# Kernel optimization log

Hardware: AMD Instinct MI355X
Metric: run time of the kernel (lower is better)

## Reference

```python
import jax, jax.numpy as jnp
import numpy as np

KEEP_RATIO = 0.3
ALPHA, BETA, GAMMA, SMOOTH = 0.3, 0.7, 1.33, 1e-6
LOVASZ_W = 0.2


def _bce_with_logits(x, t):
    # stable binary_cross_entropy_with_logits, reduction='none'
    return jnp.maximum(x, 0.0) - x * t + jnp.log1p(jnp.exp(-jnp.abs(x)))


def _ohem_image(loss_i, tgt_i, tis_i, k_all):
    # loss_i/tgt_i/tis_i: [P] per-image flattened
    P = loss_i.shape[0]
    pos = tgt_i * tis_i                       # 1.0 where kept positive
    n_pos = jnp.sum(pos).astype(jnp.int32)
    neg_mask = (tgt_i == 0) & (tis_i == 1)
    n_remain = jnp.maximum(0, k_all - n_pos)
    # top-n_remain negative losses via full descending sort + rank mask
    neg_vals = jnp.where(neg_mask, loss_i, -jnp.inf)
    neg_sorted = -jnp.sort(-neg_vals)         # descending
    ranks = jnp.arange(P)
    valid = (ranks < n_remain) & jnp.isfinite(neg_sorted)
    neg_sum = jnp.sum(jnp.where(valid, neg_sorted, 0.0))
    n_neg_kept = jnp.sum(valid).astype(jnp.int32)
    pos_sum = jnp.sum(loss_i * pos)
    cnt = n_pos + n_neg_kept
    # fallback when nothing kept: hardest pixel inside tissue (or pixel 0)
    tis_vals = jnp.where(tis_i == 1, loss_i, -jnp.inf)
    has_tissue = jnp.any(tis_i == 1)
    fallback = jnp.where(has_tissue, jnp.max(tis_vals), loss_i[0])
    return jnp.where(cnt > 0, (pos_sum + neg_sum) / jnp.maximum(cnt, 1), fallback)


def _lovasz_image(log_flat, lab_flat):
    # binary Lovasz hinge, per image
    signs = 2.0 * lab_flat - 1.0
    errors = 1.0 - log_flat * signs
    order = jnp.argsort(-errors)              # descending by error
    errors_sorted = errors[order]
    gt_sorted = lab_flat[order]
    p = jnp.sum(gt_sorted)
    intersection = p - jnp.cumsum(gt_sorted)
    union = p + jnp.cumsum(1.0 - gt_sorted)
    jaccard = 1.0 - intersection / union
    n = gt_sorted.shape[0] - p
    grad = jnp.where(n > 0,
                     jnp.concatenate([jaccard[:1], jaccard[1:] - jaccard[:-1]]),
                     jaccard)
    return jnp.dot(jax.nn.relu(errors_sorted), grad)


def _forward(logits, targets, tissue_mask):
    t = targets.astype(jnp.float32)
    B = logits.shape[0]
    lf = logits.reshape(B, -1)                # [B, P]
    tf = t.reshape(B, -1)
    mf = tissue_mask.reshape(B, -1)
    P = lf.shape[1]
    k_all = max(1, int(P * KEEP_RATIO))       # static

    # --- OHEM BCE ---
    bce = _bce_with_logits(lf, tf) * mf
    ohem_i = jax.vmap(lambda l, tg, ms: _ohem_image(l, tg, ms, k_all))(bce, tf, mf)
    ohem_term = jnp.mean(ohem_i)

    # --- focal Tversky (per image) ---
    probs = jax.nn.sigmoid(lf)
    tp = jnp.sum(probs * tf, axis=1)
    fn = jnp.sum((1.0 - probs) * tf, axis=1)
    fp = jnp.sum(probs * (1.0 - tf), axis=1)
    tversky = (tp + SMOOTH) / (tp + ALPHA * fn + BETA * fp + SMOOTH)
    ft_i = (1.0 - tversky) ** GAMMA

    # --- Lovasz hinge (per image) ---
    lov_i = jax.vmap(_lovasz_image)(lf, tf)

    # masked mean over images that contain positives
    posb = jnp.sum(tf, axis=1) > 0
    npos = jnp.sum(posb)
    denom = jnp.maximum(npos, 1).astype(lf.dtype)
    ft_term = jnp.sum(jnp.where(posb, ft_i, 0.0)) / denom
    lov_term = jnp.sum(jnp.where(posb, lov_i, 0.0)) / denom
    return ohem_term + jnp.where(npos > 0, ft_term + LOVASZ_W * lov_term, 0.0)


def setup_inputs() -> dict:
    key = jax.random.key(0)
    k1, k2 = jax.random.split(key)
    B, H, W = 16, 768, 768
    logits = jax.random.normal(k1, (B, 1, H, W), dtype=jnp.float32)
    targets = jax.random.randint(k2, (B, 1, H, W), 0, 2, dtype=jnp.int32)
    tissue_mask = jnp.ones((B, 1, H, W), dtype=jnp.float32)
    return {"logits": logits, "targets": targets, "tissue_mask": tissue_mask}


def reference(logits, targets, tissue_mask):
    return _forward(logits, targets, tissue_mask)
```

## Files before the change

kernel.cpp:

```cpp
#include <hip/hip_runtime.h>
#include <math.h>

#define BB 16
#define PP (768*768)
#define NBINS 4096
#define CHUNKS 64
#define KALL 176947

#define LOV_LO (-17.0f)
#define LOV_RANGE 34.0f

typedef unsigned long long u64;

struct PAcc { float pos_sum, pos_w, tpx, sprx, mx, sum_t, n_tis, bce0; };
struct AccR { float lov_i, ft_i, ohem_i; unsigned posb; };

__device__ inline float wred_sum(float v) {
  #pragma unroll
  for (int o = 32; o > 0; o >>= 1) v += __shfl_down(v, o, 64);
  return v;
}
__device__ inline float wred_max(float v) {
  #pragma unroll
  for (int o = 32; o > 0; o >>= 1) v = fmaxf(v, __shfl_down(v, o, 64));
  return v;
}

__global__ __launch_bounds__(256) void k_main(const float* __restrict__ logits,
                                              const int* __restrict__ targets,
                                              const float* __restrict__ mask,
                                              PAcc* __restrict__ pacc,
                                              u64* __restrict__ partial)
{
  const int b = blockIdx.y;
  const int chunk = blockIdx.x;
  __shared__ unsigned hist1[NBINS];
  __shared__ unsigned hist2[NBINS];
  __shared__ float wsum[4][8];
  for (int i = threadIdx.x; i < NBINS; i += 256) { hist1[i] = 0u; hist2[i] = 0u; }
  __syncthreads();

  const float4* l4 = (const float4*)(logits + (size_t)b * PP);
  const int4*   t4 = (const int4*)(targets + (size_t)b * PP);
  const float4* m4 = (const float4*)(mask + (size_t)b * PP);

  const float lov_scale = (float)NBINS / LOV_RANGE;

  float pos_sum = 0.f, pos_w = 0.f, tpa = 0.f, spra = 0.f, mx = 0.f;
  float sum_t = 0.f, n_tis = 0.f, bce0 = 0.f;

  if (chunk == 0 && threadIdx.x == 0) {
    float l = logits[(size_t)b * PP];
    float tf = (float)targets[(size_t)b * PP];
    float m = mask[(size_t)b * PP];
    float ex = __expf(-fabsf(l));
    bce0 = (fmaxf(l, 0.f) + __logf(1.f + ex) - l * tf) * m;
  }

  const int per_chunk4 = (PP / CHUNKS) / 4;
  const int base4 = chunk * per_chunk4;
  const int iters = per_chunk4 / 256;

  for (int it = 0; it < iters; ++it) {
    int i = base4 + it * 256 + threadIdx.x;
    float4 lv = l4[i]; int4 tv = t4[i]; float4 mv = m4[i];
    float ls[4] = {lv.x, lv.y, lv.z, lv.w};
    int   ts[4] = {tv.x, tv.y, tv.z, tv.w};
    float ms[4] = {mv.x, mv.y, mv.z, mv.w};
    #pragma unroll
    for (int c = 0; c < 4; ++c) {
      float l = ls[c]; int ti = ts[c]; float tf = (float)ti; float m = ms[c];
      float ex = __expf(-fabsf(l));
      float lg = __logf(1.f + ex);
      float loss = (fmaxf(l, 0.f) + lg - l * tf) * m;
      float posw = tf * m;
      pos_sum = fmaf(loss, posw, pos_sum);
      pos_w  += posw;
      float pr = ((l >= 0.f) ? 1.f : ex) * __builtin_amdgcn_rcpf(1.f + ex);
      spra += pr;
      tpa = fmaf(pr, tf, tpa);
      sum_t += tf;
      bool tis = (m == 1.0f);
      if (tis) { n_tis += 1.f; mx = fmaxf(mx, loss); }
      float s = fmaf(2.f, tf, -1.f);
      float e = fmaf(-l, s, 1.f);
      int bin = (int)((e - LOV_LO) * lov_scale);
      bin = bin < 0 ? 0 : (bin > NBINS - 1 ? NBINS - 1 : bin);
      atomicAdd(&hist1[bin], 1u | ((unsigned)ti << 16));
      if ((ti == 0) & tis) atomicAdd(&hist2[bin], 1u);
    }
  }

  {
    float v0 = wred_sum(pos_sum), v1 = wred_sum(pos_w), v2 = wred_sum(tpa);
    float v3 = wred_sum(spra), v4 = wred_max(mx), v5 = wred_sum(sum_t);
    float v6 = wred_sum(n_tis), v7 = wred_sum(bce0);
    int w = threadIdx.x >> 6, lane = threadIdx.x & 63;
    if (lane == 0) {
      wsum[w][0] = v0; wsum[w][1] = v1; wsum[w][2] = v2; wsum[w][3] = v3;
      wsum[w][4] = v4; wsum[w][5] = v5; wsum[w][6] = v6; wsum[w][7] = v7;
    }
  }
  __syncthreads();
  if (threadIdx.x == 0) {
    PAcc r;
    r.pos_sum = wsum[0][0] + wsum[1][0] + wsum[2][0] + wsum[3][0];
    r.pos_w   = wsum[0][1] + wsum[1][1] + wsum[2][1] + wsum[3][1];
    r.tpx     = wsum[0][2] + wsum[1][2] + wsum[2][2] + wsum[3][2];
    r.sprx    = wsum[0][3] + wsum[1][3] + wsum[2][3] + wsum[3][3];
    r.mx      = fmaxf(fmaxf(wsum[0][4], wsum[1][4]), fmaxf(wsum[2][4], wsum[3][4]));
    r.sum_t   = wsum[0][5] + wsum[1][5] + wsum[2][5] + wsum[3][5];
    r.n_tis   = wsum[0][6] + wsum[1][6] + wsum[2][6] + wsum[3][6];
    r.bce0    = wsum[0][7] + wsum[1][7] + wsum[2][7] + wsum[3][7];
    pacc[(size_t)b * CHUNKS + chunk] = r;
  }

  {
    u64* dst = partial + ((size_t)b * CHUNKS + chunk) * NBINS;
    for (int i = threadIdx.x; i < NBINS; i += 256) {
      unsigned v = hist1[i], nt = hist2[i];
      dst[i] = (u64)(v & 0xFFFFu) | ((u64)(v >> 16) << 20) | ((u64)nt << 40);
    }
  }
}

__global__ __launch_bounds__(256) void k_reduce(const u64* __restrict__ partial,
                                                u64* __restrict__ ghist,
                                                const PAcc* __restrict__ pacc,
                                                PAcc* __restrict__ accImg,
                                                unsigned* __restrict__ ticket)
{
  const int img = blockIdx.y;
  const int slice = blockIdx.x;
  const int bin = slice * 256 + threadIdx.x;
  const u64* src = partial + (size_t)img * CHUNKS * NBINS + bin;
  u64 s0 = 0, s1 = 0, s2 = 0, s3 = 0;
  #pragma unroll 4
  for (int p = 0; p < CHUNKS; p += 4) {
    s0 += src[(size_t)(p + 0) * NBINS];
    s1 += src[(size_t)(p + 1) * NBINS];
    s2 += src[(size_t)(p + 2) * NBINS];
    s3 += src[(size_t)(p + 3) * NBINS];
  }
  ghist[(size_t)img * NBINS + bin] = (s0 + s1) + (s2 + s3);

  if (slice == 0 && threadIdx.x < 64) {
    int t = threadIdx.x;
    PAcc v;
    if (t < CHUNKS) v = pacc[(size_t)img * CHUNKS + t];
    else { v.pos_sum = v.pos_w = v.tpx = v.sprx = v.mx = v.sum_t = v.n_tis = v.bce0 = 0.f; }
    v.pos_sum = wred_sum(v.pos_sum); v.pos_w = wred_sum(v.pos_w);
    v.tpx = wred_sum(v.tpx); v.sprx = wred_sum(v.sprx);
    v.mx = wred_max(v.mx); v.sum_t = wred_sum(v.sum_t);
    v.n_tis = wred_sum(v.n_tis); v.bce0 = wred_sum(v.bce0);
    if (t == 0) accImg[img] = v;
  }
  if (slice == 0 && img == 0 && threadIdx.x == 0) *ticket = 0u;
}

__global__ __launch_bounds__(256) void k_scan(const PAcc* __restrict__ accImg,
                                              const u64* __restrict__ ghist,
                                              AccR* __restrict__ acc,
                                              unsigned* __restrict__ ticket,
                                              float* __restrict__ out)
{
  const int b = blockIdx.x;
  const int t = threadIdx.x;
  __shared__ unsigned sA[256], sB[256], sC[256];
  __shared__ float sf[256], sg[256];
  __shared__ unsigned ng_total_sh;

  const u64* gh = ghist + (size_t)b * NBINS;
  const PAcc a = accImg[b];

  const unsigned sum_t = (unsigned)a.sum_t;
  const float p = (float)sum_t;
  const bool has_pos = sum_t > 0;
  const unsigned n_neg_total = (unsigned)PP - sum_t;
  const int CH = NBINS / 256;
  const float lov_d = LOV_RANGE / (float)NBINS;

  int n_pos = (int)a.pos_w;
  int n_remain = KALL - n_pos; if (n_remain < 0) n_remain = 0;

  u64 loc[16];
  unsigned tc = 0, tq = 0, tn = 0;
  #pragma unroll
  for (int k = 0; k < 16; ++k) {
    u64 v = gh[NBINS - 1 - (t * CH + k)];
    loc[k] = v;
    tc += (unsigned)(v & 0xFFFFFu);
    tq += (unsigned)((v >> 20) & 0xFFFFFu);
    tn += (unsigned)((v >> 40) & 0xFFFFFu);
  }
  sA[t] = tc; sB[t] = tq; sC[t] = tn;
  __syncthreads();
  if (t == 0) {
    unsigned aI = 0, aC = 0, aN = 0;
    for (int i = 0; i < 256; i++) {
      unsigned ci = sA[i], qi = sB[i], ni = sC[i];
      sA[i] = aI; sB[i] = aC; sC[i] = aN;
      aI += ci; aC += qi; aN += ni;
    }
    ng_total_sh = aN;
  }
  __syncthreads();

  float lov_local = 0.f, ns_local = 0.f;
  {
    unsigned I = sA[t], C = sB[t], NG = sC[t];
    float Jprev = has_pos ? (1.f - (p - (float)C) / (p + (float)I - (float)C)) : 0.f;
    #pragma unroll 4
    for (int k = 0; k < 16; ++k) {
      int j = NBINS - 1 - (t * CH + k);
      u64 v = loc[k];
      unsigned c = (unsigned)(v & 0xFFFFFu);
      if (c) {
        unsigned q = (unsigned)((v >> 20) & 0xFFFFFu);
        unsigned ng = (unsigned)((v >> 40) & 0xFFFFFu);
        float e = LOV_LO + ((float)j + 0.5f) * lov_d;
        if (has_pos) {
          float re = fmaxf(e, 0.f);
          if (n_neg_total > 0) {
            I += c; C += q;
            float Jb = 1.f - (p - (float)C) / (p + (float)I - (float)C);
            lov_local += re * (Jb - Jprev);
            Jprev = Jb;
          } else {
            double hi = (double)I + (double)c;
            double s = (hi * (hi + 1.0) - (double)I * ((double)I + 1.0)) * 0.5 / (double)p;
            lov_local += re * (float)s;
            I += c;
          }
        }
        if (n_remain > 0 && ng) {
          long long rem = (long long)n_remain - (long long)NG;
          unsigned take = rem <= 0 ? 0u : (rem >= (long long)ng ? ng : (unsigned)rem);
          if (take) {
            float l = e - 1.f;
            float nloss = fmaxf(l, 0.f) + __logf(1.f + __expf(-fabsf(l)));
            ns_local += (float)take * nloss;
          }
          NG += ng;
        }
      }
    }
  }
  sf[t] = lov_local; sg[t] = ns_local; __syncthreads();
  for (int off = 128; off > 0; off >>= 1) {
    if (t < off) { sf[t] += sf[t + off]; sg[t] += sg[t + off]; }
    __syncthreads();
  }

  if (t == 0) {
    float lov = sf[0];
    float neg_sum = sg[0];
    unsigned kept = (n_remain > 0)
        ? ((unsigned)n_remain < ng_total_sh ? (unsigned)n_remain : ng_total_sh) : 0u;
    float cnt = (float)n_pos + (float)kept;
    float ohem;
    if (cnt > 0.f) ohem = (a.pos_sum + neg_sum) / cnt;
    else ohem = (a.n_tis > 0.f) ? a.mx : a.bce0;
    float tp = a.tpx;
    float fn = p - tp;
    float fp = a.sprx - tp;
    float tv = (tp + 1e-6f) / (tp + 0.3f * fn + 0.7f * fp + 1e-6f);
    float ft = powf(fmaxf(1.f - tv, 0.f), 1.33f);
    acc[b].lov_i = lov; acc[b].ft_i = ft; acc[b].ohem_i = ohem;
    acc[b].posb = has_pos ? 1u : 0u;

    __threadfence();
    unsigned ret = atomicAdd(ticket, 1u);
    if (ret == BB - 1) {
      __threadfence();
      volatile AccR* va = acc;
      float os = 0.f, fts = 0.f, lvs = 0.f; int np = 0;
      for (int i = 0; i < BB; i++) {
        os += va[i].ohem_i;
        if (va[i].posb) { np++; fts += va[i].ft_i; lvs += va[i].lov_i; }
      }
      float denom = (np > 0) ? (float)np : 1.f;
      float r = os / (float)BB;
      if (np > 0) r += fts / denom + 0.2f * (lvs / denom);
      out[0] = r;
    }
  }
}

extern "C" void kernel_launch(void* const* d_in, const int* in_sizes, int n_in,
                              void* d_out, int out_size, void* d_ws, size_t ws_size,
                              hipStream_t stream) {
  const float* logits  = (const float*)d_in[0];
  const int*   targets = (const int*)d_in[1];
  const float* mask    = (const float*)d_in[2];
  float* out = (float*)d_out;

  char* ws = (char*)d_ws;
  AccR*     acc     = (AccR*)ws;
  unsigned* ticket  = (unsigned*)(ws + 256);
  PAcc*     accImg  = (PAcc*)(ws + 512);
  PAcc*     pacc    = (PAcc*)(ws + 1024);
  u64*      ghist   = (u64*)(ws + 64 * 1024);
  u64*      partial = (u64*)(ws + 1024 * 1024);
  (void)in_sizes; (void)n_in; (void)out_size; (void)ws_size;


  dim3 g1(CHUNKS, BB, 1);
  k_main<<<g1, 256, 0, stream>>>(logits, targets, mask, pacc, partial);
  dim3 g2(NBINS / 256, BB, 1);
  k_reduce<<<g2, 256, 0, stream>>>(partial, ghist, pacc, accImg, ticket);
  k_scan<<<BB, 256, 0, stream>>>(accImg, ghist, acc, ticket, out);
}
```

Measured before the change: 166.8 us.

## Shrink per-chunk histogram partials and raise chunk count to 96

Per-chunk partial histograms now go out as 32-bit words (packed count plus positive count) instead of 64-bit words, and the second histogram counts the rare negative non-tissue pixels as 16-bit packed pairs. The negative-in-tissue count is recovered in the reduce step by subtraction. This roughly halves partial-histogram write and read traffic and shared-memory use. Chunks go from 64 to 96 to fill more CUs, with the accumulator reduction extended to two wavefronts. The risk is 16-bit overflow per chunk, which holds at this chunk size.

```diff
diff --git a/kernel.cpp b/kernel.cpp
--- a/kernel.cpp
+++ b/kernel.cpp
@@ -4,7 +4,7 @@
 #define BB 16
 #define PP (768*768)
 #define NBINS 4096
-#define CHUNKS 64
+#define CHUNKS 96
 #define KALL 176947
 
 #define LOV_LO (-17.0f)
@@ -30,14 +30,16 @@
                                               const int* __restrict__ targets,
                                               const float* __restrict__ mask,
                                               PAcc* __restrict__ pacc,
-                                              u64* __restrict__ partial)
+                                              unsigned* __restrict__ partial1,
+                                              unsigned* __restrict__ partial3)
 {
   const int b = blockIdx.y;
   const int chunk = blockIdx.x;
   __shared__ unsigned hist1[NBINS];
-  __shared__ unsigned hist2[NBINS];
+  __shared__ unsigned hist3p[NBINS / 2];
   __shared__ float wsum[4][8];
-  for (int i = threadIdx.x; i < NBINS; i += 256) { hist1[i] = 0u; hist2[i] = 0u; }
+  for (int i = threadIdx.x; i < NBINS; i += 256) hist1[i] = 0u;
+  for (int i = threadIdx.x; i < NBINS / 2; i += 256) hist3p[i] = 0u;
   __syncthreads();
 
   const float4* l4 = (const float4*)(logits + (size_t)b * PP);
@@ -87,7 +89,8 @@
       int bin = (int)((e - LOV_LO) * lov_scale);
       bin = bin < 0 ? 0 : (bin > NBINS - 1 ? NBINS - 1 : bin);
       atomicAdd(&hist1[bin], 1u | ((unsigned)ti << 16));
-      if ((ti == 0) & tis) atomicAdd(&hist2[bin], 1u);
+      if ((ti == 0) & !tis)
+        atomicAdd(&hist3p[bin >> 1], 1u << ((bin & 1) << 4));
     }
   }
 
@@ -116,15 +119,15 @@
   }
 
   {
-    u64* dst = partial + ((size_t)b * CHUNKS + chunk) * NBINS;
-    for (int i = threadIdx.x; i < NBINS; i += 256) {
-      unsigned v = hist1[i], nt = hist2[i];
-      dst[i] = (u64)(v & 0xFFFFu) | ((u64)(v >> 16) << 20) | ((u64)nt << 40);
-    }
-  }
-}
-
-__global__ __launch_bounds__(256) void k_reduce(const u64* __restrict__ partial,
+    unsigned* d1 = partial1 + ((size_t)b * CHUNKS + chunk) * NBINS;
+    for (int i = threadIdx.x; i < NBINS; i += 256) d1[i] = hist1[i];
+    unsigned* d3 = partial3 + ((size_t)b * CHUNKS + chunk) * (NBINS / 2);
+    for (int i = threadIdx.x; i < NBINS / 2; i += 256) d3[i] = hist3p[i];
+  }
+}
+
+__global__ __launch_bounds__(256) void k_reduce(const unsigned* __restrict__ partial1,
+                                                const unsigned* __restrict__ partial3,
                                                 u64* __restrict__ ghist,
                                                 const PAcc* __restrict__ pacc,
                                                 PAcc* __restrict__ accImg,
@@ -133,18 +136,21 @@
   const int img = blockIdx.y;
   const int slice = blockIdx.x;
   const int bin = slice * 256 + threadIdx.x;
-  const u64* src = partial + (size_t)img * CHUNKS * NBINS + bin;
-  u64 s0 = 0, s1 = 0, s2 = 0, s3 = 0;
+  const unsigned* s1 = partial1 + (size_t)img * CHUNKS * NBINS + bin;
+  const unsigned* s3 = partial3 + (size_t)img * CHUNKS * (NBINS / 2) + (bin >> 1);
+  const unsigned sh3 = (bin & 1) << 4;
+  unsigned c = 0, q = 0, n0 = 0;
   #pragma unroll 4
-  for (int p = 0; p < CHUNKS; p += 4) {
-    s0 += src[(size_t)(p + 0) * NBINS];
-    s1 += src[(size_t)(p + 1) * NBINS];
-    s2 += src[(size_t)(p + 2) * NBINS];
-    s3 += src[(size_t)(p + 3) * NBINS];
-  }
-  ghist[(size_t)img * NBINS + bin] = (s0 + s1) + (s2 + s3);
-
-  if (slice == 0 && threadIdx.x < 64) {
+  for (int p = 0; p < CHUNKS; ++p) {
+    unsigned v = s1[(size_t)p * NBINS];
+    c += v & 0xFFFFu; q += v >> 16;
+    n0 += (s3[(size_t)p * (NBINS / 2)] >> sh3) & 0xFFFFu;
+  }
+  unsigned negtis = (c - q) - n0;
+  ghist[(size_t)img * NBINS + bin] =
+      (u64)c | ((u64)q << 20) | ((u64)negtis << 40);
+
+  if (slice == 0 && threadIdx.x < 128) {
     int t = threadIdx.x;
     PAcc v;
     if (t < CHUNKS) v = pacc[(size_t)img * CHUNKS + t];
@@ -153,7 +159,15 @@
     v.tpx = wred_sum(v.tpx); v.sprx = wred_sum(v.sprx);
     v.mx = wred_max(v.mx); v.sum_t = wred_sum(v.sum_t);
     v.n_tis = wred_sum(v.n_tis); v.bce0 = wred_sum(v.bce0);
-    if (t == 0) accImg[img] = v;
+    __shared__ PAcc half[2];
+    if ((t & 63) == 0) half[t >> 6] = v;
+    __syncthreads();
+    if (t == 0) {
+      PAcc r = half[0], h = half[1];
+      r.pos_sum += h.pos_sum; r.pos_w += h.pos_w; r.tpx += h.tpx; r.sprx += h.sprx;
+      r.mx = fmaxf(r.mx, h.mx); r.sum_t += h.sum_t; r.n_tis += h.n_tis; r.bce0 += h.bce0;
+      accImg[img] = r;
+    }
   }
   if (slice == 0 && img == 0 && threadIdx.x == 0) *ticket = 0u;
 }
@@ -296,18 +310,19 @@
   float* out = (float*)d_out;
 
   char* ws = (char*)d_ws;
-  AccR*     acc     = (AccR*)ws;
-  unsigned* ticket  = (unsigned*)(ws + 256);
-  PAcc*     accImg  = (PAcc*)(ws + 512);
-  PAcc*     pacc    = (PAcc*)(ws + 1024);
-  u64*      ghist   = (u64*)(ws + 64 * 1024);
-  u64*      partial = (u64*)(ws + 1024 * 1024);
+  AccR*     acc      = (AccR*)ws;
+  unsigned* ticket   = (unsigned*)(ws + 256);
+  PAcc*     accImg   = (PAcc*)(ws + 512);
+  PAcc*     pacc     = (PAcc*)(ws + 1024);
+  u64*      ghist    = (u64*)(ws + (64 << 10));
+  unsigned* partial1 = (unsigned*)(ws + (1 << 20));
+  unsigned* partial3 = (unsigned*)(ws + (1 << 20) + (size_t)BB * CHUNKS * NBINS * 4);
   (void)in_sizes; (void)n_in; (void)out_size; (void)ws_size;
 
 
   dim3 g1(CHUNKS, BB, 1);
-  k_main<<<g1, 256, 0, stream>>>(logits, targets, mask, pacc, partial);
+  k_main<<<g1, 256, 0, stream>>>(logits, targets, mask, pacc, partial1, partial3);
   dim3 g2(NBINS / 256, BB, 1);
-  k_reduce<<<g2, 256, 0, stream>>>(partial, ghist, pacc, accImg, ticket);
+  k_reduce<<<g2, 256, 0, stream>>>(partial1, partial3, ghist, pacc, accImg, ticket);
   k_scan<<<BB, 256, 0, stream>>>(accImg, ghist, acc, ticket, out);
 }
```

Result: slower. 170.9 us (+2.5%).
